# Optimization experiments

Measured on AMD Instinct MI355X. Metric: run time of the kernel, lower is better.

Reference implementation:

```python
import jax, jax.numpy as jnp
import numpy as np
from jax import lax

E = 5      # num experts
K = 3      # used (top-k)
B, C, H, W = 16, 128, 64, 64
DW = 2 * C   # NAFBlock DW_Expand=2
FFN = 2 * C  # NAFBlock FFN_Expand=2
EPS = 1e-6   # NAFNet LayerNorm2d eps


def setup_inputs() -> dict:
    key = jax.random.key(0)
    ks = jax.random.split(key, 12)
    r = lambda i, shape, s=0.05: jax.random.normal(ks[i], shape, jnp.float32) * s
    return dict(
        feat=jax.random.normal(ks[0], (B, C, H, W), jnp.float32),
        weights=jax.random.uniform(ks[1], (B, E), jnp.float32, minval=0.01, maxval=1.0),
        ln1_w=jnp.ones((E, C), jnp.float32), ln1_b=jnp.zeros((E, C), jnp.float32),
        conv1_w=r(2, (E, DW, C)), conv1_b=jnp.zeros((E, DW), jnp.float32),
        conv2_w=r(3, (E, DW, 1, 3, 3)), conv2_b=jnp.zeros((E, DW), jnp.float32),
        sca_w=r(4, (E, C, C)), sca_b=jnp.zeros((E, C), jnp.float32),
        conv3_w=r(5, (E, C, C)), conv3_b=jnp.zeros((E, C), jnp.float32),
        ln2_w=jnp.ones((E, C), jnp.float32), ln2_b=jnp.zeros((E, C), jnp.float32),
        conv4_w=r(6, (E, FFN, C)), conv4_b=jnp.zeros((E, FFN), jnp.float32),
        conv5_w=r(7, (E, C, FFN // 2)), conv5_b=jnp.zeros((E, C), jnp.float32),
        beta=r(8, (E, C), 1.0), gamma=r(9, (E, C), 1.0),
    )


def _ln2d(x, w, b):
    # channel-wise LayerNorm over C for each (b, h, w)
    mu = jnp.mean(x, 1, keepdims=True)
    v = jnp.mean((x - mu) ** 2, 1, keepdims=True)
    return (x - mu) * lax.rsqrt(v + EPS) * w[None, :, None, None] + b[None, :, None, None]


def _c1x1(x, w, b):
    return jnp.einsum('oc,bchw->bohw', w, x) + b[None, :, None, None]


def _sg(x):  # SimpleGate
    a, g = jnp.split(x, 2, axis=1)
    return a * g


def _naf(x, ln1w, ln1b, w1, b1, w2, b2, scaw, scab, w3, b3, ln2w, ln2b, w4, b4, w5, b5, beta, gamma):
    y = _c1x1(_ln2d(x, ln1w, ln1b), w1, b1)                      # [B,2C,H,W]
    y = lax.conv_general_dilated(y, w2, (1, 1), 'SAME',
                                 feature_group_count=DW,
                                 dimension_numbers=('NCHW', 'OIHW', 'NCHW')) + b2[None, :, None, None]
    y = _sg(y)                                                    # [B,C,H,W]
    s = jnp.einsum('oc,bc->bo', scaw, jnp.mean(y, (2, 3))) + scab # SCA
    y = y * s[:, :, None, None]
    y = _c1x1(y, w3, b3)
    x = x + y * beta[None, :, None, None]
    z = _c1x1(_sg(_c1x1(_ln2d(x, ln2w, ln2b), w4, b4)), w5, b5)
    return x + z * gamma[None, :, None, None]


def reference(feat, weights, ln1_w, ln1_b, conv1_w, conv1_b, conv2_w, conv2_b,
              sca_w, sca_b, conv3_w, conv3_b, ln2_w, ln2_b, conv4_w, conv4_b,
              conv5_w, conv5_b, beta, gamma):
    b = feat.shape[0]
    tw, ti = lax.top_k(weights, K)
    tw = tw / jnp.sum(tw, 1, keepdims=True)
    # gate[b,e] = normalized topk weight if expert e selected for sample b, else 0
    gate = jnp.zeros((b, E), feat.dtype).at[jnp.arange(b)[:, None], ti].set(tw)
    counts = jnp.bincount(ti.ravel(), length=E)
    expert_outs = jax.vmap(lambda *p: _naf(feat, *p))(
        ln1_w, ln1_b, conv1_w, conv1_b, conv2_w, conv2_b, sca_w, sca_b,
        conv3_w, conv3_b, ln2_w, ln2_b, conv4_w, conv4_b, conv5_w, conv5_b, beta, gamma)
    outputs = jnp.einsum('ebchw,be->bchw', expert_outs, gate)
    return (outputs, counts, weights)
```

## Files before the change

kernel.cpp:

```cpp
#include <hip/hip_runtime.h>

#define EN 5
#define KT 3
#define BB 16
#define CC 128
#define HWP 4096
#define DWC 256
#define NPAIR 48
#define EPSLN 1e-6f
#define HR 10
#define HPX 100
#define TSTRIDE 106

typedef float f32x4 __attribute__((ext_vector_type(4)));
typedef __bf16 bf16x8 __attribute__((ext_vector_type(8)));

__device__ __forceinline__ float bf2f(ushort u) {
  union { unsigned int u; float f; } v; v.u = ((unsigned int)u) << 16; return v.f;
}
__device__ __forceinline__ uint cvtpk(float lo, float hi) {
  uint r;
  asm("v_cvt_pk_bf16_f32 %0, %1, %2" : "=v"(r) : "v"(lo), "v"(hi));
  return r;
}
__device__ __forceinline__ ushort f2bf(float f) {
  union { float f; unsigned int u; } v; v.f = f;
  unsigned int r = v.u + 0x7FFFu + ((v.u >> 16) & 1u);
  return (ushort)(r >> 16);
}
__device__ __forceinline__ ushort f2bf1(float f) {
  return (ushort)(cvtpk(f, f) & 0xffffu);
}
__device__ __forceinline__ ushort4 pack4(float a, float b, float c, float d) {
  union { uint2 u; ushort4 s; } v;
  v.u.x = cvtpk(a, b);
  v.u.y = cvtpk(c, d);
  return v.s;
}

__global__ void gate_kernel(const float* __restrict__ weights, float* __restrict__ gate_w,
                            int* __restrict__ pair_e, float* __restrict__ out_counts,
                            float* __restrict__ out_weights, float* __restrict__ mean_raw) {
  __shared__ int sel[NPAIR];
  int tid = threadIdx.x;
  if (tid < BB) {
    float w[EN];
    for (int e = 0; e < EN; e++) w[e] = weights[tid * EN + e];
    int ch[KT]; float cv[KT]; float sum = 0.f;
    for (int j = 0; j < KT; j++) {
      int best = -1; float bv = -3.4e38f;
      for (int e = 0; e < EN; e++) {
        bool used = false;
        for (int q = 0; q < j; q++) if (ch[q] == e) used = true;
        if (!used && w[e] > bv) { bv = w[e]; best = e; }
      }
      ch[j] = best; cv[j] = bv; sum += bv;
    }
    float inv = 1.f / sum;
    for (int j = 0; j < KT; j++) {
      gate_w[tid * KT + j] = cv[j] * inv;
      pair_e[tid * KT + j] = ch[j];
      sel[tid * KT + j] = ch[j];
    }
  }
  for (int i = tid; i < NPAIR * CC; i += 256) mean_raw[i] = 0.f;
  __syncthreads();
  if (tid < EN) {
    int cnt = 0;
    for (int i = 0; i < NPAIR; i++) if (sel[i] == tid) cnt++;
    out_counts[tid] = (float)cnt;
  }
  if (tid < BB * EN) out_weights[tid] = weights[tid];
}

__global__ void fold_kernel(const float* __restrict__ conv1_w, const float* __restrict__ conv1_b,
                            const float* __restrict__ ln1_w, const float* __restrict__ ln1_b,
                            const float* __restrict__ conv4_w, const float* __restrict__ conv4_b,
                            const float* __restrict__ ln2_w, const float* __restrict__ ln2_b,
                            const float* __restrict__ conv3_b, const float* __restrict__ beta,
                            ushort* __restrict__ W1eff, float* __restrict__ b1eff,
                            ushort* __restrict__ W4eff, float* __restrict__ b4eff,
                            float* __restrict__ b3eff) {
  int gid = blockIdx.x * 256 + threadIdx.x;
  if (gid < 2 * EN * DWC) {
    int which = gid / (EN * DWC), rem = gid % (EN * DWC);
    int e = rem / DWC, o = rem % DWC;
    const float* src = (which ? conv4_w : conv1_w) + (size_t)(e * DWC + o) * CC;
    const float* lw = (which ? ln2_w : ln1_w) + e * CC;
    const float* lb = (which ? ln2_b : ln1_b) + e * CC;
    float bacc = (which ? conv4_b : conv1_b)[e * DWC + o];
    ushort* dst = (which ? W4eff : W1eff) + (size_t)(e * DWC + o) * CC;
    for (int c = 0; c < CC; c++) {
      float wv = src[c];
      dst[c] = f2bf(wv * lw[c]);
      bacc += wv * lb[c];
    }
    (which ? b4eff : b1eff)[e * DWC + o] = bacc;
  } else if (gid < 2 * EN * DWC + EN * CC) {
    int x = gid - 2 * EN * DWC;
    b3eff[x] = beta[x] * conv3_b[x];
  }
}

__global__ void fold2_kernel(const float* __restrict__ conv5_w, const float* __restrict__ conv5_b,
                             const float* __restrict__ gamma, const float* __restrict__ gate_w,
                             const int* __restrict__ pair_e,
                             ushort* __restrict__ W5eff, float* __restrict__ b5tot) {
  int gid = blockIdx.x * 256 + threadIdx.x;
  const int nW = NPAIR * CC * CC / 8;
  if (gid < nW) {
    int base = gid * 8;
    int p = base >> 14, rem = base & 16383;
    int o = rem >> 7, k0 = rem & 127;
    int e = pair_e[p];
    float sc = gamma[e * CC + o] * gate_w[p];
    const float* src = conv5_w + ((size_t)e * CC + o) * CC + k0;
    ushort* dst = W5eff + ((size_t)p * CC + o) * CC + k0;
    for (int q = 0; q < 8; q++) dst[q] = f2bf(src[q] * sc);
  } else if (gid < nW + BB * CC) {
    int x = gid - nW;
    int b = x >> 7, o = x & 127;
    float s = 0.f;
    for (int j = 0; j < KT; j++) {
      int p = b * KT + j, e = pair_e[p];
      s += gate_w[p] * gamma[e * CC + o] * conv5_b[e * CC + o];
    }
    b5tot[x] = s;
  }
}

__global__ __launch_bounds__(256) void ln1_kernel(const float* __restrict__ feat,
                                                  ushort* __restrict__ xhatT,
                                                  ushort* __restrict__ featT) {
  __shared__ float tile[CC * 64];
  __shared__ float pS[4][64], pS2[4][64], bcM[64], bcR[64];
  int bimg = blockIdx.x >> 6;
  int n0 = (blockIdx.x & 63) * 64;
  int tid = threadIdx.x;
  const float* src = feat + (size_t)bimg * CC * HWP + n0;
#pragma unroll
  for (int i = 0; i < 8; i++) {
    int ch = tid + i * 256;
    int row = ch >> 4, c16 = ch & 15;
    *(float4*)&tile[row * 64 + c16 * 4] = *(const float4*)(src + (size_t)row * HWP + c16 * 4);
  }
  __syncthreads();
  int lane = tid & 63, w = tid >> 6;
  float s = 0.f, s2 = 0.f;
#pragma unroll
  for (int i = 0; i < 32; i++) {
    float v = tile[(w * 32 + i) * 64 + lane];
    s += v; s2 += v * v;
  }
  pS[w][lane] = s; pS2[w][lane] = s2;
  __syncthreads();
  if (w == 0) {
    float t1 = pS[0][lane] + pS[1][lane] + pS[2][lane] + pS[3][lane];
    float t2 = pS2[0][lane] + pS2[1][lane] + pS2[2][lane] + pS2[3][lane];
    float mu = t1 * (1.f / CC);
    float var = t2 * (1.f / CC) - mu * mu;
    bcM[lane] = mu; bcR[lane] = rsqrtf(var + EPSLN);
  }
  __syncthreads();
  float mu = bcM[lane], r = bcR[lane];
  size_t obase = ((size_t)bimg * HWP + n0 + lane) * CC + w * 32;
#pragma unroll
  for (int i = 0; i < 4; i++) {
    float v[8];
#pragma unroll
    for (int q = 0; q < 8; q++) v[q] = tile[(w * 32 + i * 8 + q) * 64 + lane];
    *(ushort4*)(featT + obase + i * 8)     = pack4(v[0], v[1], v[2], v[3]);
    *(ushort4*)(featT + obase + i * 8 + 4) = pack4(v[4], v[5], v[6], v[7]);
    *(ushort4*)(xhatT + obase + i * 8)     = pack4((v[0]-mu)*r, (v[1]-mu)*r, (v[2]-mu)*r, (v[3]-mu)*r);
    *(ushort4*)(xhatT + obase + i * 8 + 4) = pack4((v[4]-mu)*r, (v[5]-mu)*r, (v[6]-mu)*r, (v[7]-mu)*r);
  }
}

__device__ __forceinline__ void stage_tile(const ushort* __restrict__ g, ushort* lds, int tid) {
#pragma unroll
  for (int i = 0; i < 8; i++) {
    int d = (tid + i * 256) * 16;
    int row = d >> 8;
    uint4 v = *(const uint4*)((const char*)g + d);
    *(uint4*)((char*)lds + (d ^ ((row & 7) << 4))) = v;
  }
}
__device__ __forceinline__ bf16x8 ldfrag(const ushort* lds, int row, int kb) {
  return *(const bf16x8*)((const char*)lds + row * 256 + (kb ^ ((row & 7) << 4)));
}
__device__ __forceinline__ void stage8(ushort* st, int px, int o, ushort4 v) {
  *(ushort4*)((char*)st + px * 256 + ((o * 2) ^ ((px & 7) << 4))) = v;
}
__device__ __forceinline__ uint4 ldstage16(const ushort* st, int px, int ck) {
  return *(const uint4*)((const char*)st + px * 256 + ((ck * 16) ^ ((px & 7) << 4)));
}

__global__ __launch_bounds__(256, 3) void c1dw_kernel(
    const ushort* __restrict__ W1eff, const float* __restrict__ b1eff,
    const ushort* __restrict__ xhatT,
    const float* __restrict__ conv2_w, const float* __restrict__ conv2_b,
    const int* __restrict__ pair_e, int pair_lo,
    ushort* __restrict__ yT, float* __restrict__ mean_raw) {
  __shared__ __align__(16) char smem[DWC * TSTRIDE * 2];
  int ts = blockIdx.x;
  int pc = blockIdx.z, p = pair_lo + pc, e = pair_e[p];
  int img = p / KT;
  int th = (ts >> 3) * 8, tw = (ts & 7) * 8;
  int tid = threadIdx.x, lane = tid & 63, w = tid >> 6;
  int fr = lane & 15, qf = lane >> 4;

#pragma unroll
  for (int i = 0; i < 7; i++) {
    int idx = tid + i * 256;
    if (idx < HPX * 16) {
      int r = idx >> 4, seg = idx & 15;
      int hy = r / HR, hx = r - hy * HR;
      int hh = th + hy - 1, ww = tw + hx - 1;
      int hc = min(max(hh, 0), 63), wc = min(max(ww, 0), 63);
      uint4 v = *(const uint4*)(xhatT + ((size_t)img * HWP + hc * 64 + wc) * CC + seg * 8);
      *(uint4*)(smem + r * 256 + ((seg * 16) ^ ((r & 7) << 4))) = v;
    }
  }
  __syncthreads();

  f32x4 acc[7][4] = {};
#pragma unroll
  for (int ks = 0; ks < 4; ks++) {
    bf16x8 bfr[4];
#pragma unroll
    for (int mf = 0; mf < 4; mf++)
      bfr[mf] = *(const bf16x8*)(W1eff + (size_t)(e * DWC + w * 64 + mf * 16 + fr) * CC + ks * 32 + qf * 8);
#pragma unroll
    for (int nf = 0; nf < 7; nf++) {
      bf16x8 a = ldfrag((const ushort*)smem, nf * 16 + fr, ks * 64 + qf * 16);
#pragma unroll
      for (int mf = 0; mf < 4; mf++)
        acc[nf][mf] = __builtin_amdgcn_mfma_f32_16x16x32_bf16(a, bfr[mf], acc[nf][mf], 0, 0, 0);
    }
  }
  float bias[4];
#pragma unroll
  for (int mf = 0; mf < 4; mf++) bias[mf] = b1eff[e * DWC + w * 64 + mf * 16 + fr];
  __syncthreads();

  ushort* Th = (ushort*)smem;
  int px0q = qf * 4;
#pragma unroll
  for (int nf = 0; nf < 7; nf++) {
    int px = nf * 16 + px0q;
    if (px < HPX) {
#pragma unroll
      for (int mf = 0; mf < 4; mf++) {
        int ch = w * 64 + mf * 16 + fr;
        f32x4 v = acc[nf][mf];
        float bb = bias[mf];
        uint u0 = cvtpk(v.x + bb, v.y + bb);
        uint u1 = cvtpk(v.z + bb, v.w + bb);
        ushort* dst = Th + ch * TSTRIDE + px;
        *(uint*)dst = u0;
        *(uint*)(dst + 2) = u1;
      }
    }
  }
  __syncthreads();

  int cp = tid & 127, ph2 = tid >> 7;
  bool zTop = (ph2 == 0) && (th == 0);
  bool zBot = (ph2 == 1) && (th == 56);
  bool leftE = (tw == 0), rightE = (tw == 56);
  const float* wAp = conv2_w + ((size_t)e * DWC + cp) * 9;
  const float* wGp = conv2_w + ((size_t)(e * DWC + CC) + cp) * 9;
  float wA9[9], wG9[9];
#pragma unroll
  for (int k = 0; k < 9; k++) { wA9[k] = wAp[k]; wG9[k] = wGp[k]; }
  float ba = conv2_b[e * DWC + cp], bg = conv2_b[e * DWC + CC + cp];

  auto loadrowz = [&](float* dst, const ushort* pp, bool zrow) {
    if (zrow) {
#pragma unroll
      for (int q = 0; q < 10; q++) dst[q] = 0.f;
    } else {
#pragma unroll
      for (int q = 0; q < 5; q++) {
        uint u = *(const uint*)(pp + q * 2);
        dst[q * 2]     = bf2f((ushort)(u & 0xffffu));
        dst[q * 2 + 1] = bf2f((ushort)(u >> 16));
      }
      if (leftE) dst[0] = 0.f;
      if (rightE) dst[9] = 0.f;
    }
  };
  auto comp3 = [&](const float* w9, const float* r0, const float* r1, const float* r2, float* out) {
#pragma unroll
    for (int ox = 0; ox < 8; ox++) {
      float a = r0[ox] * w9[0];
      a = fmaf(r0[ox + 1], w9[1], a); a = fmaf(r0[ox + 2], w9[2], a);
      a = fmaf(r1[ox],     w9[3], a); a = fmaf(r1[ox + 1], w9[4], a);
      a = fmaf(r1[ox + 2], w9[5], a);
      a = fmaf(r2[ox],     w9[6], a); a = fmaf(r2[ox + 1], w9[7], a);
      a = fmaf(r2[ox + 2], w9[8], a);
      out[ox] = a;
    }
  };

  float win[3][10];
  float outv[4][8];
  {
    const ushort* rA = Th + cp * TSTRIDE + ph2 * 40;
    loadrowz(win[0], rA, zTop); loadrowz(win[1], rA + 10, false); loadrowz(win[2], rA + 20, false);
    comp3(wA9, win[0], win[1], win[2], outv[0]);
    loadrowz(win[0], rA + 30, false);
    comp3(wA9, win[1], win[2], win[0], outv[1]);
    loadrowz(win[1], rA + 40, false);
    comp3(wA9, win[2], win[0], win[1], outv[2]);
    loadrowz(win[2], rA + 50, zBot);
    comp3(wA9, win[0], win[1], win[2], outv[3]);
  }
  uint ypk[16];
  float csum = 0.f;
  {
    const ushort* rG = Th + (cp + 128) * TSTRIDE + ph2 * 40;
    float gtmp[8];
    loadrowz(win[0], rG, zTop); loadrowz(win[1], rG + 10, false); loadrowz(win[2], rG + 20, false);
#pragma unroll
    for (int oy = 0; oy < 4; oy++) {
      if (oy == 1) { loadrowz(win[0], rG + 30, false); }
      if (oy == 2) { loadrowz(win[1], rG + 40, false); }
      if (oy == 3) { loadrowz(win[2], rG + 50, zBot); }
      const float* r0 = (oy == 0) ? win[0] : (oy == 1) ? win[1] : (oy == 2) ? win[2] : win[0];
      const float* r1 = (oy == 0) ? win[1] : (oy == 1) ? win[2] : (oy == 2) ? win[0] : win[1];
      const float* r2 = (oy == 0) ? win[2] : (oy == 1) ? win[0] : (oy == 2) ? win[1] : win[2];
      comp3(wG9, r0, r1, r2, gtmp);
#pragma unroll
      for (int ox = 0; ox < 8; ox += 2) {
        float y0 = (outv[oy][ox]     + ba) * (gtmp[ox]     + bg);
        float y1 = (outv[oy][ox + 1] + ba) * (gtmp[ox + 1] + bg);
        csum += y0 + y1;
        ypk[oy * 4 + (ox >> 1)] = cvtpk(y0, y1);
      }
    }
  }
  __syncthreads();

  float* psum = (float*)(smem + 16384);
#pragma unroll
  for (int oy = 0; oy < 4; oy++)
#pragma unroll
    for (int ox = 0; ox < 8; ox++) {
      int opx = (ph2 * 4 + oy) * 8 + ox;
      uint pkv = ypk[oy * 4 + (ox >> 1)];
      ushort val = (ox & 1) ? (ushort)(pkv >> 16) : (ushort)(pkv & 0xffffu);
      *(ushort*)(smem + opx * 256 + ((cp * 2) ^ ((opx & 7) << 4))) = val;
    }
  psum[tid] = csum;
  __syncthreads();
#pragma unroll
  for (int i = 0; i < 4; i++) {
    int idx = tid + i * 256;
    int opx = idx >> 4, ck = idx & 15;
    uint4 v = *(const uint4*)(smem + opx * 256 + ((ck * 16) ^ ((opx & 7) << 4)));
    int n = (th + (opx >> 3)) * 64 + tw + (opx & 7);
    *(uint4*)((char*)(yT + ((size_t)pc * HWP + n) * CC) + ck * 16) = v;
  }
  if (tid < CC) {
    atomicAdd(&mean_raw[p * CC + tid], psum[tid] + psum[CC + tid]);
  }
}

__global__ void sca_w3fold_kernel(const float* __restrict__ mean_raw,
                                  const float* __restrict__ sca_w, const float* __restrict__ sca_b,
                                  const float* __restrict__ conv3_w, const float* __restrict__ beta,
                                  const int* __restrict__ pair_e, int pair_lo,
                                  ushort* __restrict__ W3eff) {
  __shared__ float m[CC];
  __shared__ float sv[CC];
  int pc = blockIdx.x, p = pair_lo + pc, e = pair_e[p];
  int tid = threadIdx.x;
  if (tid < CC) m[tid] = mean_raw[p * CC + tid] * (1.f / HWP);
  __syncthreads();
  if (tid < CC) {
    const float* wr = sca_w + (size_t)(e * CC + tid) * CC;
    float acc = sca_b[e * CC + tid];
#pragma unroll 8
    for (int c = 0; c < CC; c++) acc = fmaf(wr[c], m[c], acc);
    sv[tid] = acc;
  }
  __syncthreads();
#pragma unroll
  for (int i = 0; i < 8; i++) {
    int idx = tid + i * 256;
    int o = idx >> 4, k0 = (idx & 15) * 8;
    float bt = beta[e * CC + o];
    const float* src = conv3_w + ((size_t)e * CC + o) * CC + k0;
    ushort* dst = W3eff + ((size_t)pc * CC + o) * CC + k0;
#pragma unroll
    for (int q = 0; q < 8; q++) dst[q] = f2bf(src[q] * sv[k0 + q] * bt);
  }
}

__global__ __launch_bounds__(256, 2) void c34_kernel(
    const ushort* __restrict__ W3eff, const float* __restrict__ b3eff,
    const ushort* __restrict__ W4eff, const float* __restrict__ b4eff,
    const ushort* __restrict__ yT, const ushort* __restrict__ featT,
    const int* __restrict__ pair_e, int pair_lo,
    ushort* __restrict__ x1T, ushort* __restrict__ g5T) {
  __shared__ ushort Ws[CC * CC];
  __shared__ ushort As[CC * CC];
  __shared__ float2 red2[256];
  int pc = blockIdx.z, p = pair_lo + pc, e = pair_e[p];
  int img = p / KT;
  int n0 = blockIdx.x * 128;
  int tid = threadIdx.x, lane = tid & 63, w = tid >> 6;
  int wr = w >> 1, wc = w & 1, fr = lane & 15, kb0 = (lane >> 4) * 16, og = (lane >> 4) * 4;

  stage_tile(W3eff + (size_t)pc * CC * CC, Ws, tid);
  stage_tile(yT + ((size_t)pc * HWP + n0) * CC, As, tid);
  __syncthreads();
  f32x4 acc3[4][4] = {};
#pragma unroll
  for (int ks = 0; ks < 4; ks++) {
    bf16x8 a[4], bb[4];
#pragma unroll
    for (int m = 0; m < 4; m++) a[m] = ldfrag(Ws, wr * 64 + m * 16 + fr, ks * 64 + kb0);
#pragma unroll
    for (int n = 0; n < 4; n++) bb[n] = ldfrag(As, wc * 64 + n * 16 + fr, ks * 64 + kb0);
#pragma unroll
    for (int m = 0; m < 4; m++)
#pragma unroll
      for (int n = 0; n < 4; n++)
        acc3[m][n] = __builtin_amdgcn_mfma_f32_16x16x32_bf16(a[m], bb[n], acc3[m][n], 0, 0, 0);
  }
  float s[4] = {}, s2[4] = {};
#pragma unroll
  for (int m = 0; m < 4; m++) {
    int o = wr * 64 + m * 16 + og;
    float4 bvv = *(const float4*)&b3eff[e * CC + o];
#pragma unroll
    for (int n = 0; n < 4; n++) {
      int px = wc * 64 + n * 16 + fr;
      ushort4 f4 = *(const ushort4*)(featT + ((size_t)img * HWP + n0 + px) * CC + o);
      f32x4 v = acc3[m][n];
      v.x += bf2f(f4.x) + bvv.x; v.y += bf2f(f4.y) + bvv.y;
      v.z += bf2f(f4.z) + bvv.z; v.w += bf2f(f4.w) + bvv.w;
      acc3[m][n] = v;
      s[n] += v.x + v.y + v.z + v.w;
      s2[n] += v.x * v.x + v.y * v.y + v.z * v.z + v.w * v.w;
    }
  }
#pragma unroll
  for (int n = 0; n < 4; n++) {
    s[n] += __shfl_xor(s[n], 16, 64); s[n] += __shfl_xor(s[n], 32, 64);
    s2[n] += __shfl_xor(s2[n], 16, 64); s2[n] += __shfl_xor(s2[n], 32, 64);
  }
  if (lane < 16) {
#pragma unroll
    for (int n = 0; n < 4; n++) {
      float2 v; v.x = s[n]; v.y = s2[n];
      red2[wr * 128 + wc * 64 + n * 16 + fr] = v;
    }
  }
  __syncthreads();
  float mu[4], rs[4];
#pragma unroll
  for (int n = 0; n < 4; n++) {
    int px = wc * 64 + n * 16 + fr;
    float2 r0 = red2[px], r1 = red2[128 + px];
    float m_ = (r0.x + r1.x) * (1.f / CC);
    float var = (r0.y + r1.y) * (1.f / CC) - m_ * m_;
    mu[n] = m_; rs[n] = rsqrtf(var + EPSLN);
  }
#pragma unroll
  for (int m = 0; m < 4; m++) {
    int o = wr * 64 + m * 16 + og;
#pragma unroll
    for (int n = 0; n < 4; n++) {
      int px = wc * 64 + n * 16 + fr;
      f32x4 v = acc3[m][n];
      stage8(Ws, px, o, pack4(v.x, v.y, v.z, v.w));
      stage8(As, px, o, pack4((v.x - mu[n]) * rs[n], (v.y - mu[n]) * rs[n],
                              (v.z - mu[n]) * rs[n], (v.w - mu[n]) * rs[n]));
    }
  }
  __syncthreads();
#pragma unroll
  for (int i = 0; i < 8; i++) {
    int idx = tid + i * 256;
    int px = idx >> 4, ck = idx & 15;
    *(uint4*)((char*)(x1T + ((size_t)pc * HWP + n0 + px) * CC) + ck * 16) = ldstage16(Ws, px, ck);
  }
  __syncthreads();
  stage_tile(W4eff + (size_t)e * DWC * CC, Ws, tid);
  __syncthreads();
  f32x4 accA[4][4] = {};
#pragma unroll
  for (int ks = 0; ks < 4; ks++) {
    bf16x8 a[4], bb[4];
#pragma unroll
    for (int m = 0; m < 4; m++) a[m] = ldfrag(Ws, wr * 64 + m * 16 + fr, ks * 64 + kb0);
#pragma unroll
    for (int n = 0; n < 4; n++) bb[n] = ldfrag(As, wc * 64 + n * 16 + fr, ks * 64 + kb0);
#pragma unroll
    for (int m = 0; m < 4; m++)
#pragma unroll
      for (int n = 0; n < 4; n++)
        accA[m][n] = __builtin_amdgcn_mfma_f32_16x16x32_bf16(a[m], bb[n], accA[m][n], 0, 0, 0);
  }
  uint pA[4][4][2];
#pragma unroll
  for (int m = 0; m < 4; m++) {
    int o = wr * 64 + m * 16 + og;
    float4 ba4 = *(const float4*)&b4eff[e * DWC + o];
#pragma unroll
    for (int n = 0; n < 4; n++) {
      f32x4 v = accA[m][n];
      pA[m][n][0] = cvtpk(v.x + ba4.x, v.y + ba4.y);
      pA[m][n][1] = cvtpk(v.z + ba4.z, v.w + ba4.w);
    }
  }
  __syncthreads();
  stage_tile(W4eff + ((size_t)e * DWC + CC) * CC, Ws, tid);
  __syncthreads();
  f32x4 accG[4][4] = {};
#pragma unroll
  for (int ks = 0; ks < 4; ks++) {
    bf16x8 a[4], bb[4];
#pragma unroll
    for (int m = 0; m < 4; m++) a[m] = ldfrag(Ws, wr * 64 + m * 16 + fr, ks * 64 + kb0);
#pragma unroll
    for (int n = 0; n < 4; n++) bb[n] = ldfrag(As, wc * 64 + n * 16 + fr, ks * 64 + kb0);
#pragma unroll
    for (int m = 0; m < 4; m++)
#pragma unroll
      for (int n = 0; n < 4; n++)
        accG[m][n] = __builtin_amdgcn_mfma_f32_16x16x32_bf16(a[m], bb[n], accG[m][n], 0, 0, 0);
  }
  __syncthreads();
#pragma unroll
  for (int m = 0; m < 4; m++) {
    int o = wr * 64 + m * 16 + og;
    float4 bg4 = *(const float4*)&b4eff[e * DWC + CC + o];
#pragma unroll
    for (int n = 0; n < 4; n++) {
      int px = wc * 64 + n * 16 + fr;
      f32x4 vg = accG[m][n];
      uint u0 = pA[m][n][0], u1 = pA[m][n][1];
      float g0 = bf2f((ushort)(u0 & 0xffffu)) * (vg.x + bg4.x);
      float g1 = bf2f((ushort)(u0 >> 16))     * (vg.y + bg4.y);
      float g2 = bf2f((ushort)(u1 & 0xffffu)) * (vg.z + bg4.z);
      float g3 = bf2f((ushort)(u1 >> 16))     * (vg.w + bg4.w);
      stage8(As, px, o, pack4(g0, g1, g2, g3));
    }
  }
  __syncthreads();
#pragma unroll
  for (int i = 0; i < 8; i++) {
    int idx = tid + i * 256;
    int px = idx >> 4, ck = idx & 15;
    *(uint4*)((char*)(g5T + ((size_t)pc * HWP + n0 + px) * CC) + ck * 16) = ldstage16(As, px, ck);
  }
}

__global__ __launch_bounds__(256, 2) void conv5_kernel(
    const ushort* __restrict__ W5eff, const float* __restrict__ b5tot,
    const ushort* __restrict__ g5T, const ushort* __restrict__ x1,
    const float* __restrict__ gate_w, int pair_lo, float* __restrict__ out) {
  __shared__ ushort Ws[CC * CC];
  __shared__ ushort As[CC * CC];
  int sl = blockIdx.z;
  int n0 = blockIdx.x * 128;
  int b = pair_lo / KT + sl;
  int tid = threadIdx.x, lane = tid & 63, w = tid >> 6;
  int wr = w >> 1, wc = w & 1;
  int fr = lane & 15, kb0 = (lane >> 4) * 16, og = (lane >> 4) * 4;
  f32x4 acc[4][4] = {};
  for (int j = 0; j < KT; j++) {
    int pc = sl * KT + j, p = pair_lo + pc;
    __syncthreads();
    stage_tile(W5eff + (size_t)p * CC * CC, Ws, tid);
    stage_tile(g5T + ((size_t)pc * HWP + n0) * CC, As, tid);
    __syncthreads();
#pragma unroll
    for (int ks = 0; ks < 4; ks++) {
      bf16x8 a[4], bfr[4];
#pragma unroll
      for (int m = 0; m < 4; m++) a[m] = ldfrag(Ws, wr * 64 + m * 16 + fr, ks * 64 + kb0);
#pragma unroll
      for (int n = 0; n < 4; n++) bfr[n] = ldfrag(As, wc * 64 + n * 16 + fr, ks * 64 + kb0);
#pragma unroll
      for (int m = 0; m < 4; m++)
#pragma unroll
        for (int n = 0; n < 4; n++)
          acc[m][n] = __builtin_amdgcn_mfma_f32_16x16x32_bf16(a[m], bfr[n], acc[m][n], 0, 0, 0);
    }
  }
  float gw0 = gate_w[pair_lo + sl * KT + 0];
  float gw1 = gate_w[pair_lo + sl * KT + 1];
  float gw2 = gate_w[pair_lo + sl * KT + 2];
  __syncthreads();
  ushort* Ct = As;
#pragma unroll
  for (int m = 0; m < 4; m++) {
    int o = wr * 64 + m * 16 + og;
    float4 bt = *(const float4*)&b5tot[b * CC + o];
#pragma unroll
    for (int n = 0; n < 4; n++) {
      int px = wc * 64 + n * 16 + fr;
      f32x4 v = acc[m][n];
      float r0 = v.x + bt.x, r1 = v.y + bt.y, r2 = v.z + bt.z, r3 = v.w + bt.w;
      size_t xoff = ((size_t)(sl * KT) * HWP + n0 + px) * CC + o;
      ushort4 xa = *(const ushort4*)(x1 + xoff);
      ushort4 xb = *(const ushort4*)(x1 + xoff + (size_t)HWP * CC);
      ushort4 xc = *(const ushort4*)(x1 + xoff + 2 * (size_t)HWP * CC);
      r0 += gw0 * bf2f(xa.x) + gw1 * bf2f(xb.x) + gw2 * bf2f(xc.x);
      r1 += gw0 * bf2f(xa.y) + gw1 * bf2f(xb.y) + gw2 * bf2f(xc.y);
      r2 += gw0 * bf2f(xa.z) + gw1 * bf2f(xb.z) + gw2 * bf2f(xc.z);
      r3 += gw0 * bf2f(xa.w) + gw1 * bf2f(xb.w) + gw2 * bf2f(xc.w);
      *(ushort*)((char*)Ct + (o+0) * 256 + ((px*2) ^ (((o+0) & 7) << 4))) = f2bf1(r0);
      *(ushort*)((char*)Ct + (o+1) * 256 + ((px*2) ^ (((o+1) & 7) << 4))) = f2bf1(r1);
      *(ushort*)((char*)Ct + (o+2) * 256 + ((px*2) ^ (((o+2) & 7) << 4))) = f2bf1(r2);
      *(ushort*)((char*)Ct + (o+3) * 256 + ((px*2) ^ (((o+3) & 7) << 4))) = f2bf1(r3);
    }
  }
  __syncthreads();
  int o = tid >> 1, ph = (tid & 1) * 64;
  float* orow = out + ((size_t)(b * CC + o)) * HWP + n0 + ph;
  int swz = (o & 7) << 4;
#pragma unroll
  for (int i = 0; i < 8; i++) {
    const ushort* lp = (const ushort*)((const char*)Ct + o * 256 + ((ph * 2 + i * 16) ^ swz));
    float4 f0, f1;
    f0.x = bf2f(lp[0]); f0.y = bf2f(lp[1]); f0.z = bf2f(lp[2]); f0.w = bf2f(lp[3]);
    f1.x = bf2f(lp[4]); f1.y = bf2f(lp[5]); f1.z = bf2f(lp[6]); f1.w = bf2f(lp[7]);
    *(float4*)(orow + i * 8) = f0;
    *(float4*)(orow + i * 8 + 4) = f1;
  }
}

extern "C" void kernel_launch(void* const* d_in, const int* in_sizes, int n_in,
                              void* d_out, int out_size, void* d_ws, size_t ws_size,
                              hipStream_t stream) {
  const float* feat    = (const float*)d_in[0];
  const float* weights = (const float*)d_in[1];
  const float* ln1_w   = (const float*)d_in[2];
  const float* ln1_b   = (const float*)d_in[3];
  const float* conv1_w = (const float*)d_in[4];
  const float* conv1_b = (const float*)d_in[5];
  const float* conv2_w = (const float*)d_in[6];
  const float* conv2_b = (const float*)d_in[7];
  const float* sca_w   = (const float*)d_in[8];
  const float* sca_b   = (const float*)d_in[9];
  const float* conv3_w = (const float*)d_in[10];
  const float* conv3_b = (const float*)d_in[11];
  const float* ln2_w   = (const float*)d_in[12];
  const float* ln2_b   = (const float*)d_in[13];
  const float* conv4_w = (const float*)d_in[14];
  const float* conv4_b = (const float*)d_in[15];
  const float* conv5_w = (const float*)d_in[16];
  const float* conv5_b = (const float*)d_in[17];
  const float* beta    = (const float*)d_in[18];
  const float* gamma   = (const float*)d_in[19];

  float* out = (float*)d_out;
  float* out_counts = out + (size_t)BB * CC * HWP;
  float* out_weights = out_counts + EN;

  char* base = (char*)d_ws;
  size_t off = 0;
  auto carveU = [&](size_t n) -> ushort* { ushort* p = (ushort*)(base + off); off += n * 2; return p; };
  auto carveF = [&](size_t n) -> float* { float* p = (float*)(base + off); off += n * 4; return p; };

  ushort* W1eff = carveU((size_t)EN * DWC * CC);
  ushort* W4eff = carveU((size_t)EN * DWC * CC);
  ushort* W5eff = carveU((size_t)NPAIR * CC * CC);
  ushort* W3eff = carveU((size_t)NPAIR * CC * CC);
  float* b1eff  = carveF(EN * DWC);
  float* b4eff  = carveF(EN * DWC);
  float* b3eff  = carveF(EN * CC);
  float* b5tot  = carveF(BB * CC);
  float* gate_w = carveF(64);
  int*   pair_e = (int*)carveF(64);
  float* mean_raw = carveF(NPAIR * CC);
  ushort* xhatT = carveU((size_t)BB * HWP * CC);
  ushort* featT = carveU((size_t)BB * HWP * CC);

  const size_t per_pair = (size_t)3 * HWP * CC * 2;
  int ns = 16;
  while (ns > 1 && off + (size_t)ns * KT * per_pair > ws_size) ns >>= 1;
  size_t pr = (size_t)ns * KT;
  ushort* y_T  = carveU(pr * HWP * CC);
  ushort* x1_T = carveU(pr * HWP * CC);
  ushort* g5_T = carveU(pr * HWP * CC);

  gate_kernel<<<1, 256, 0, stream>>>(weights, gate_w, pair_e, out_counts, out_weights, mean_raw);
  fold_kernel<<<13, 256, 0, stream>>>(conv1_w, conv1_b, ln1_w, ln1_b,
                                      conv4_w, conv4_b, ln2_w, ln2_b,
                                      conv3_b, beta, W1eff, b1eff, W4eff, b4eff, b3eff);
  fold2_kernel<<<393, 256, 0, stream>>>(conv5_w, conv5_b, gamma, gate_w, pair_e, W5eff, b5tot);
  ln1_kernel<<<BB * 64, 256, 0, stream>>>(feat, xhatT, featT);

  for (int s0 = 0; s0 < BB; s0 += ns) {
    int np = ns * KT, plo = s0 * KT;
    c1dw_kernel<<<dim3(64, 1, np), 256, 0, stream>>>(W1eff, b1eff, xhatT, conv2_w, conv2_b,
                                                     pair_e, plo, y_T, mean_raw);
    sca_w3fold_kernel<<<np, 256, 0, stream>>>(mean_raw, sca_w, sca_b, conv3_w, beta,
                                              pair_e, plo, W3eff);
    c34_kernel<<<dim3(32, 1, np), 256, 0, stream>>>(W3eff, b3eff, W4eff, b4eff,
                                                    y_T, featT, pair_e, plo, x1_T, g5_T);
    conv5_kernel<<<dim3(32, 1, ns), 256, 0, stream>>>(W5eff, b5tot, g5_T, x1_T,
                                                      gate_w, plo, out);
  }
}
```

Before: 200.1 us.

## Split c1dw kernel over two channel halves to raise occupancy

Each c1dw block now computes only 64 of the 128 SimpleGate output channels (the matching a/g conv1 channel pairs), with a new grid y dimension of 2. This halves the LDS transposition buffer, the accumulator registers and per-thread depthwise work, and the launch bound rises to 4 waves per SIMD. The cost is that the 10x10 input halo tile gets loaded and the 1x1-conv B operand gets re-read twice per tile, with twice as many blocks and atomics.

```diff
diff --git a/kernel.cpp b/kernel.cpp
--- a/kernel.cpp
+++ b/kernel.cpp
@@ -195,14 +195,15 @@
   return *(const uint4*)((const char*)st + px * 256 + ((ck * 16) ^ ((px & 7) << 4)));
 }
 
-__global__ __launch_bounds__(256, 3) void c1dw_kernel(
+__global__ __launch_bounds__(256, 4) void c1dw_kernel(
     const ushort* __restrict__ W1eff, const float* __restrict__ b1eff,
     const ushort* __restrict__ xhatT,
     const float* __restrict__ conv2_w, const float* __restrict__ conv2_b,
     const int* __restrict__ pair_e, int pair_lo,
     ushort* __restrict__ yT, float* __restrict__ mean_raw) {
-  __shared__ __align__(16) char smem[DWC * TSTRIDE * 2];
+  __shared__ __align__(16) char smem[CC * TSTRIDE * 2];
   int ts = blockIdx.x;
+  int h = blockIdx.y;
   int pc = blockIdx.z, p = pair_lo + pc, e = pair_e[p];
   int img = p / KT;
   int th = (ts >> 3) * 8, tw = (ts & 7) * 8;
@@ -223,24 +224,26 @@
   }
   __syncthreads();
 
-  f32x4 acc[7][4] = {};
+  int gchbase = ((w >> 1) * CC) + h * 64 + (w & 1) * 32;
+  int lcbase  = ((w >> 1) * 64) + (w & 1) * 32;
+  f32x4 acc[7][2] = {};
 #pragma unroll
   for (int ks = 0; ks < 4; ks++) {
-    bf16x8 bfr[4];
-#pragma unroll
-    for (int mf = 0; mf < 4; mf++)
-      bfr[mf] = *(const bf16x8*)(W1eff + (size_t)(e * DWC + w * 64 + mf * 16 + fr) * CC + ks * 32 + qf * 8);
+    bf16x8 bfr[2];
+#pragma unroll
+    for (int mf = 0; mf < 2; mf++)
+      bfr[mf] = *(const bf16x8*)(W1eff + (size_t)(e * DWC + gchbase + mf * 16 + fr) * CC + ks * 32 + qf * 8);
 #pragma unroll
     for (int nf = 0; nf < 7; nf++) {
       bf16x8 a = ldfrag((const ushort*)smem, nf * 16 + fr, ks * 64 + qf * 16);
 #pragma unroll
-      for (int mf = 0; mf < 4; mf++)
+      for (int mf = 0; mf < 2; mf++)
         acc[nf][mf] = __builtin_amdgcn_mfma_f32_16x16x32_bf16(a, bfr[mf], acc[nf][mf], 0, 0, 0);
     }
   }
-  float bias[4];
-#pragma unroll
-  for (int mf = 0; mf < 4; mf++) bias[mf] = b1eff[e * DWC + w * 64 + mf * 16 + fr];
+  float bias[2];
+#pragma unroll
+  for (int mf = 0; mf < 2; mf++) bias[mf] = b1eff[e * DWC + gchbase + mf * 16 + fr];
   __syncthreads();
 
   ushort* Th = (ushort*)smem;
@@ -250,13 +253,13 @@
     int px = nf * 16 + px0q;
     if (px < HPX) {
 #pragma unroll
-      for (int mf = 0; mf < 4; mf++) {
-        int ch = w * 64 + mf * 16 + fr;
+      for (int mf = 0; mf < 2; mf++) {
+        int lc = lcbase + mf * 16 + fr;
         f32x4 v = acc[nf][mf];
         float bb = bias[mf];
         uint u0 = cvtpk(v.x + bb, v.y + bb);
         uint u1 = cvtpk(v.z + bb, v.w + bb);
-        ushort* dst = Th + ch * TSTRIDE + px;
+        ushort* dst = Th + lc * TSTRIDE + px;
         *(uint*)dst = u0;
         *(uint*)(dst + 2) = u1;
       }
@@ -264,27 +267,27 @@
   }
   __syncthreads();
 
-  int cp = tid & 127, ph2 = tid >> 7;
-  bool zTop = (ph2 == 0) && (th == 0);
-  bool zBot = (ph2 == 1) && (th == 56);
+  int cp = lane, q = w;
+  bool zT = (th == 0), zB = (th == 56);
   bool leftE = (tw == 0), rightE = (tw == 56);
-  const float* wAp = conv2_w + ((size_t)e * DWC + cp) * 9;
-  const float* wGp = conv2_w + ((size_t)(e * DWC + CC) + cp) * 9;
+  int sgch = h * 64 + cp;
+  const float* wAp = conv2_w + ((size_t)e * DWC + sgch) * 9;
+  const float* wGp = conv2_w + ((size_t)(e * DWC + CC) + sgch) * 9;
   float wA9[9], wG9[9];
 #pragma unroll
   for (int k = 0; k < 9; k++) { wA9[k] = wAp[k]; wG9[k] = wGp[k]; }
-  float ba = conv2_b[e * DWC + cp], bg = conv2_b[e * DWC + CC + cp];
+  float ba = conv2_b[e * DWC + sgch], bg = conv2_b[e * DWC + CC + sgch];
 
   auto loadrowz = [&](float* dst, const ushort* pp, bool zrow) {
     if (zrow) {
 #pragma unroll
-      for (int q = 0; q < 10; q++) dst[q] = 0.f;
+      for (int qq = 0; qq < 10; qq++) dst[qq] = 0.f;
     } else {
 #pragma unroll
-      for (int q = 0; q < 5; q++) {
-        uint u = *(const uint*)(pp + q * 2);
-        dst[q * 2]     = bf2f((ushort)(u & 0xffffu));
-        dst[q * 2 + 1] = bf2f((ushort)(u >> 16));
+      for (int qq = 0; qq < 5; qq++) {
+        uint u = *(const uint*)(pp + qq * 2);
+        dst[qq * 2]     = bf2f((ushort)(u & 0xffffu));
+        dst[qq * 2 + 1] = bf2f((ushort)(u >> 16));
       }
       if (leftE) dst[0] = 0.f;
       if (rightE) dst[9] = 0.f;
@@ -304,66 +307,61 @@
   };
 
   float win[3][10];
-  float outv[4][8];
+  float outA[2][8], outG[2][8];
   {
-    const ushort* rA = Th + cp * TSTRIDE + ph2 * 40;
-    loadrowz(win[0], rA, zTop); loadrowz(win[1], rA + 10, false); loadrowz(win[2], rA + 20, false);
-    comp3(wA9, win[0], win[1], win[2], outv[0]);
-    loadrowz(win[0], rA + 30, false);
-    comp3(wA9, win[1], win[2], win[0], outv[1]);
-    loadrowz(win[1], rA + 40, false);
-    comp3(wA9, win[2], win[0], win[1], outv[2]);
-    loadrowz(win[2], rA + 50, zBot);
-    comp3(wA9, win[0], win[1], win[2], outv[3]);
-  }
-  uint ypk[16];
+    const ushort* rA = Th + cp * TSTRIDE + q * 20;
+    loadrowz(win[0], rA, (q == 0) && zT);
+    loadrowz(win[1], rA + 10, false);
+    loadrowz(win[2], rA + 20, false);
+    comp3(wA9, win[0], win[1], win[2], outA[0]);
+    loadrowz(win[0], rA + 30, (q == 3) && zB);
+    comp3(wA9, win[1], win[2], win[0], outA[1]);
+  }
+  {
+    const ushort* rG = Th + (64 + cp) * TSTRIDE + q * 20;
+    loadrowz(win[0], rG, (q == 0) && zT);
+    loadrowz(win[1], rG + 10, false);
+    loadrowz(win[2], rG + 20, false);
+    comp3(wG9, win[0], win[1], win[2], outG[0]);
+    loadrowz(win[0], rG + 30, (q == 3) && zB);
+    comp3(wG9, win[1], win[2], win[0], outG[1]);
+  }
+  uint ypk[8];
   float csum = 0.f;
-  {
-    const ushort* rG = Th + (cp + 128) * TSTRIDE + ph2 * 40;
-    float gtmp[8];
-    loadrowz(win[0], rG, zTop); loadrowz(win[1], rG + 10, false); loadrowz(win[2], rG + 20, false);
-#pragma unroll
-    for (int oy = 0; oy < 4; oy++) {
-      if (oy == 1) { loadrowz(win[0], rG + 30, false); }
-      if (oy == 2) { loadrowz(win[1], rG + 40, false); }
-      if (oy == 3) { loadrowz(win[2], rG + 50, zBot); }
-      const float* r0 = (oy == 0) ? win[0] : (oy == 1) ? win[1] : (oy == 2) ? win[2] : win[0];
-      const float* r1 = (oy == 0) ? win[1] : (oy == 1) ? win[2] : (oy == 2) ? win[0] : win[1];
-      const float* r2 = (oy == 0) ? win[2] : (oy == 1) ? win[0] : (oy == 2) ? win[1] : win[2];
-      comp3(wG9, r0, r1, r2, gtmp);
-#pragma unroll
-      for (int ox = 0; ox < 8; ox += 2) {
-        float y0 = (outv[oy][ox]     + ba) * (gtmp[ox]     + bg);
-        float y1 = (outv[oy][ox + 1] + ba) * (gtmp[ox + 1] + bg);
-        csum += y0 + y1;
-        ypk[oy * 4 + (ox >> 1)] = cvtpk(y0, y1);
-      }
-    }
-  }
-  __syncthreads();
-
-  float* psum = (float*)(smem + 16384);
-#pragma unroll
-  for (int oy = 0; oy < 4; oy++)
+#pragma unroll
+  for (int r = 0; r < 2; r++)
+#pragma unroll
+    for (int ox = 0; ox < 8; ox += 2) {
+      float y0 = (outA[r][ox]     + ba) * (outG[r][ox]     + bg);
+      float y1 = (outA[r][ox + 1] + ba) * (outG[r][ox + 1] + bg);
+      csum += y0 + y1;
+      ypk[r * 4 + (ox >> 1)] = cvtpk(y0, y1);
+    }
+  __syncthreads();
+
+  float* psum = (float*)(smem + 8192);
+#pragma unroll
+  for (int r = 0; r < 2; r++)
 #pragma unroll
     for (int ox = 0; ox < 8; ox++) {
-      int opx = (ph2 * 4 + oy) * 8 + ox;
-      uint pkv = ypk[oy * 4 + (ox >> 1)];
+      int opx = (q * 2 + r) * 8 + ox;
+      uint pkv = ypk[r * 4 + (ox >> 1)];
       ushort val = (ox & 1) ? (ushort)(pkv >> 16) : (ushort)(pkv & 0xffffu);
-      *(ushort*)(smem + opx * 256 + ((cp * 2) ^ ((opx & 7) << 4))) = val;
+      *(ushort*)(smem + opx * 128 + ((cp * 2) ^ ((opx & 7) << 4))) = val;
     }
   psum[tid] = csum;
   __syncthreads();
 #pragma unroll
-  for (int i = 0; i < 4; i++) {
+  for (int i = 0; i < 2; i++) {
     int idx = tid + i * 256;
-    int opx = idx >> 4, ck = idx & 15;
-    uint4 v = *(const uint4*)(smem + opx * 256 + ((ck * 16) ^ ((opx & 7) << 4)));
+    int opx = idx >> 3, ck = idx & 7;
+    uint4 v = *(const uint4*)(smem + opx * 128 + ((ck * 16) ^ ((opx & 7) << 4)));
     int n = (th + (opx >> 3)) * 64 + tw + (opx & 7);
-    *(uint4*)((char*)(yT + ((size_t)pc * HWP + n) * CC) + ck * 16) = v;
-  }
-  if (tid < CC) {
-    atomicAdd(&mean_raw[p * CC + tid], psum[tid] + psum[CC + tid]);
+    *(uint4*)((char*)(yT + ((size_t)pc * HWP + n) * CC + h * 64) + ck * 16) = v;
+  }
+  if (tid < 64) {
+    float s = psum[tid] + psum[64 + tid] + psum[128 + tid] + psum[192 + tid];
+    atomicAdd(&mean_raw[p * CC + h * 64 + tid], s);
   }
 }
 
@@ -700,7 +698,7 @@
 
   for (int s0 = 0; s0 < BB; s0 += ns) {
     int np = ns * KT, plo = s0 * KT;
-    c1dw_kernel<<<dim3(64, 1, np), 256, 0, stream>>>(W1eff, b1eff, xhatT, conv2_w, conv2_b,
+    c1dw_kernel<<<dim3(64, 2, np), 256, 0, stream>>>(W1eff, b1eff, xhatT, conv2_w, conv2_b,
                                                      pair_e, plo, y_T, mean_raw);
     sca_w3fold_kernel<<<np, 256, 0, stream>>>(mean_raw, sca_w, sca_b, conv3_w, beta,
                                               pair_e, plo, W3eff);
```

New measurement: 186.9 us (median of 3 runs). 1.07x faster.
